# Optimization experiments

Hardware: AMD Instinct MI355X
Metric: run time of the kernel (lower is better)

## Reference

```python
import jax, jax.numpy as jnp
import numpy as np

K, N, NE, NI, MA, IN, B = 8, 512, 256, 256, 3, 128, 1024
H, UNFOLDS = 0.04, 6
DT = H / UNFOLDS
STATE = NE * MA + NI * MA + NE + NI + N  # 2560


def inv_softplus(x):
    return float(np.log(np.expm1(x)))


def piecewise_sigmoid(x, S_a=0.9, S_c=0.0):
    a = S_a / 2.0
    c = S_c
    k = 0.5 / (1.0 - 2.0 * a)  # = 5.0 for S_a=0.9
    x1, x2, x3, x4 = c + a - 1.0, c - a, c + a, c + 1.0 - a
    quad_rise = k * (x - x1) * (x - x1)
    linear = x - c + 0.5
    quad_cap = 1.0 - k * (x - x4) * (x - x4)
    out = jnp.where(x < x1, 0.0, quad_rise)
    out = jnp.where(x >= x2, linear, out)
    out = jnp.where(x > x3, quad_cap, out)
    out = jnp.where(x > x4, 1.0, out)
    return out


def setup_inputs():
    key = jax.random.key(0)
    ks = jax.random.split(key, 6)
    m = (jax.random.uniform(ks[0], (K, N, N)) > 0.5).astype(jnp.float32)  # sparsity masks
    W_raw = jax.random.normal(ks[1], (K, N, N)) * np.float32(np.sqrt(2.0 / N)) * m
    W_in = jax.random.normal(ks[2], (K, N, IN)) * 0.1
    lo, hi = inv_softplus(0.25), inv_softplus(10.0)
    taus = jnp.asarray([lo + (hi - lo) * ai / (MA - 1) for ai in range(MA)], dtype=jnp.float32)
    log_tau_a = jnp.tile(taus[None, None, :], (K, NE, 1))
    return {
        "inputs": jax.random.normal(ks[3], (B, IN), dtype=jnp.float32),
        "state": jax.random.uniform(ks[4], (K, B, STATE), dtype=jnp.float32),
        "W_raw": W_raw,
        "sparsity_masks": m,
        "W_in": W_in,
        "a_0": jnp.full((K, N), 0.35, jnp.float32),
        "log_tau_d": jnp.full((K, N), inv_softplus(0.1), jnp.float32),
        "log_tau_a_E": log_tau_a,
        "log_c_E": jnp.full((K, NE, MA), -3.0, jnp.float32),
        "c_0_E": jnp.zeros((K, NE, MA), jnp.float32),
        "log_tau_a_I": log_tau_a,
        "log_c_I": jnp.full((K, NI, MA), -3.0, jnp.float32),
        "c_0_I": jnp.zeros((K, NI, MA), jnp.float32),
        "log_tau_b_rec_E": jnp.full((K, NE), inv_softplus(1.0), jnp.float32),
        "log_tau_b_rel_E": jnp.full((K, NE), inv_softplus(0.25), jnp.float32),
        "log_tau_b_rec_I": jnp.full((K, NI), inv_softplus(1.0), jnp.float32),
        "log_tau_b_rel_I": jnp.full((K, NI), inv_softplus(0.25), jnp.float32),
        "readout_ids": jnp.zeros((K,), dtype=jnp.int32),  # 0=synaptic,1=rate,2=dendritic
    }


def _forward(inputs, state, W_raw, sparsity_masks, W_in, a_0, log_tau_d,
             log_tau_a_E, log_c_E, c_0_E, log_tau_a_I, log_c_I, c_0_I,
             log_tau_b_rec_E, log_tau_b_rel_E, log_tau_b_rec_I, log_tau_b_rel_I,
             readout_ids):
    sp = jax.nn.softplus
    # unpack flat state (K,B,STATE)
    i0 = NE * MA; i1 = i0 + NI * MA; i2 = i1 + NE; i3 = i2 + NI
    aE = state[:, :, :i0].reshape(K, B, NE, MA)
    aI = state[:, :, i0:i1].reshape(K, B, NI, MA)
    bE = state[:, :, i1:i2]          # (K,B,NE)
    bI = state[:, :, i2:i3]          # (K,B,NI)
    x = state[:, :, i3:]             # (K,B,N)
    # Dale-constrained effective recurrent weights
    W_pos = sp(W_raw)
    W_eff = jnp.concatenate([W_pos[:, :, :NE], -W_pos[:, :, NE:]], axis=2) * sparsity_masks
    # time-constant gains
    gx = DT / sp(log_tau_d)[:, None]                    # (K,1,N)
    gaE = DT / sp(log_tau_a_E)[:, None]                 # (K,1,NE,MA)
    gaI = DT / sp(log_tau_a_I)[:, None]
    cE = sp(log_c_E)[:, None]                           # (K,1,NE,MA)
    cI = sp(log_c_I)[:, None]
    grecE = (DT / sp(log_tau_b_rec_E))[:, None]         # (K,1,NE)
    grelE = (DT / sp(log_tau_b_rel_E))[:, None]
    grecI = (DT / sp(log_tau_b_rec_I))[:, None]
    grelI = (DT / sp(log_tau_b_rel_I))[:, None]
    in_cur = jnp.einsum('kni,bi->kbn', W_in, inputs)    # constant across unfolds

    def rate_syn(aE, aI, bE, bI, x):
        thr = a_0[:, None] + jnp.concatenate(
            [jnp.sum(aE + c_0_E[:, None], axis=-1),
             jnp.sum(aI + c_0_I[:, None], axis=-1)], axis=-1)
        r = piecewise_sigmoid(x - thr)                  # (K,B,N)
        s = r * jnp.concatenate([bE, bI], axis=-1)      # depression-scaled output
        return r, s

    def step(carry, _):
        aE, aI, bE, bI, x = carry
        r, s = rate_syn(aE, aI, bE, bI, x)
        rE, rI = r[..., :NE], r[..., NE:]
        syn = jnp.einsum('knm,kbm->kbn', W_eff, s) + in_cur
        x = (x + gx * syn) / (1.0 + gx)                 # semi-implicit Euler
        aE = (aE + gaE * cE * rE[..., None]) / (1.0 + gaE)
        aI = (aI + gaI * cI * rI[..., None]) / (1.0 + gaI)
        bE = (bE + grecE) / (1.0 + grecE + grelE * rE)
        bI = (bI + grecI) / (1.0 + grecI + grelI * rI)
        return (aE, aI, bE, bI, x), None

    (aE, aI, bE, bI, x), _ = jax.lax.scan(step, (aE, aI, bE, bI, x), None, length=UNFOLDS)
    r, s = rate_syn(aE, aI, bE, bI, x)
    rid = readout_ids[:, None, None]
    out = jnp.where(rid == 0, s, jnp.where(rid == 1, r, x))
    new_state = jnp.concatenate(
        [aE.reshape(K, B, -1), aI.reshape(K, B, -1), bE, bI, x], axis=-1)
    return out, new_state


def reference(inputs, state, W_raw, sparsity_masks, W_in, a_0, log_tau_d,
              log_tau_a_E, log_c_E, c_0_E, log_tau_a_I, log_c_I, c_0_I,
              log_tau_b_rec_E, log_tau_b_rel_E, log_tau_b_rec_I, log_tau_b_rel_I,
              readout_ids):
    return _forward(inputs, state, W_raw, sparsity_masks, W_in, a_0, log_tau_d,
                    log_tau_a_E, log_c_E, c_0_E, log_tau_a_I, log_c_I, c_0_I,
                    log_tau_b_rec_E, log_tau_b_rel_E, log_tau_b_rec_I, log_tau_b_rel_I,
                    readout_ids)
```

## Files before the change

### kernel.cpp

```cpp
#include <hip/hip_runtime.h>
#include <stdint.h>

#define K_ 8
#define N_ 512
#define NE_ 256
#define MA_ 3
#define IN_ 128
#define B_ 1024
#define STATE_ 2560
#define UNFOLDS_ 6
#define DT_ (0.04f / 6.0f)

typedef __attribute__((ext_vector_type(8))) short short8;
typedef __attribute__((ext_vector_type(4))) float floatx4;

__device__ __forceinline__ float b2f(uint16_t u) {
    union { uint32_t i; float f; } v; v.i = ((uint32_t)u) << 16; return v.f;
}
__device__ __forceinline__ uint16_t f2b(float f) {
    union { float f; uint32_t i; } v; v.f = f;
    uint32_t i = v.i;
    uint32_t r = i + 0x7FFFu + ((i >> 16) & 1u);
    return (uint16_t)(r >> 16);
}
__device__ __forceinline__ uint32_t pack2(uint16_t lo, uint16_t hi) {
    return (uint32_t)lo | ((uint32_t)hi << 16);
}
__device__ __forceinline__ float loadf(const void* p, size_t i, int f32) {
    return f32 ? ((const float*)p)[i] : b2f(((const uint16_t*)p)[i]);
}
__device__ __forceinline__ float spf(float x) {
    return (x > 20.f) ? x : log1pf(expf(x));
}
__device__ __forceinline__ float psig(float x) {
    float t1 = x + 0.55f;
    float q1 = 5.f * t1 * t1;
    float t2 = x - 0.55f;
    float q2 = 1.f - 5.f * t2 * t2;
    float out = (x < -0.55f) ? 0.f : q1;
    out = (x >= -0.45f) ? (x + 0.5f) : out;
    out = (x > 0.45f) ? q2 : out;
    out = (x > 0.55f) ? 1.f : out;
    return out;
}

__global__ void srnn_detect_kernel(const uint16_t* canary, int* flag) {
    __shared__ int cnt;
    if (threadIdx.x == 0) cnt = 0;
    __syncthreads();
    int bad = 0;
    for (int i = threadIdx.x; i < 4096; i += 256) {
        uint16_t u = canary[i];
        int e = (u >> 7) & 0xFF;
        if (e >= 0xC0) bad++;
    }
    atomicAdd(&cnt, bad);
    __syncthreads();
    if (threadIdx.x == 0) flag[0] = (cnt >= 16) ? 1 : 0;
}

__global__ void srnn_params_kernel(
    const void* a0, const void* ltd,
    const void* ltaE, const void* lcE, const void* c0E,
    const void* ltaI, const void* lcI, const void* c0I,
    const void* lbrecE, const void* lbrelE,
    const void* lbrecI, const void* lbrelI,
    const int* flag, float* P)
{
    const int f = flag[0];
    int idx = blockIdx.x * 256 + threadIdx.x;
    if (idx >= K_ * N_) return;
    int n = idx & (N_ - 1);
    int k = idx >> 9;
    float gx = DT_ / spf(loadf(ltd, idx, f));
    float thr0 = loadf(a0, idx, f);

    const void *lta, *lc, *c0, *lbrec, *lbrel;
    int nn;
    if (n < NE_) { nn = n;        lta = ltaE; lc = lcE; c0 = c0E; lbrec = lbrecE; lbrel = lbrelE; }
    else         { nn = n - NE_;  lta = ltaI; lc = lcI; c0 = c0I; lbrec = lbrecI; lbrel = lbrelI; }
    int base3 = (k * NE_ + nn) * MA_;
    int base1 = k * NE_ + nn;

    float amul[3], ainv[3];
    #pragma unroll
    for (int j = 0; j < 3; ++j) {
        float ga = DT_ / spf(loadf(lta, base3 + j, f));
        float c  = spf(loadf(lc, base3 + j, f));
        amul[j] = ga * c;
        ainv[j] = 1.f / (1.f + ga);
        thr0 += loadf(c0, base3 + j, f);
    }
    float grec = DT_ / spf(loadf(lbrec, base1, f));
    float grel = DT_ / spf(loadf(lbrel, base1, f));

    const int KN = K_ * N_;
    P[0*KN + idx] = gx;
    P[1*KN + idx] = 1.f / (1.f + gx);
    P[2*KN + idx] = thr0;
    P[3*KN + idx] = grec;
    P[4*KN + idx] = grel;
    P[5*KN + idx] = amul[0]; P[6*KN + idx] = amul[1]; P[7*KN + idx] = amul[2];
    P[8*KN + idx] = ainv[0]; P[9*KN + idx] = ainv[1]; P[10*KN + idx] = ainv[2];
}

__global__ __launch_bounds__(256) void srnn_wsw_kernel(
    const void* __restrict__ Wraw, const void* __restrict__ mask,
    const int* __restrict__ flag, uint16_t* __restrict__ Wsw)
{
    __shared__ float tile[16 * 516];
    const int f = flag[0];
    const int nt = blockIdx.x, k = blockIdx.y, t = threadIdx.x;
    const size_t base = (size_t)k * N_ * N_ + (size_t)nt * 16 * N_;
    #pragma unroll
    for (int i = 0; i < 32; ++i) {
        int idx = i * 256 + t;
        int row = idx >> 9, m = idx & 511;
        size_t gi = base + (size_t)row * N_ + m;
        float w = spf(loadf(Wraw, gi, f)) * loadf(mask, gi, f);
        if (m >= NE_) w = -w;
        tile[row * 516 + m] = w;
    }
    __syncthreads();
    uint16_t* outb = Wsw + ((size_t)k * 32 + nt) * (16 * 64 * 8);
    #pragma unroll
    for (int i = 0; i < 4; ++i) {
        int id = i * 256 + t;
        int ks = id >> 6, L = id & 63;
        int row = L & 15, quad = L >> 4;
        const float* src = &tile[row * 516 + ks * 32 + quad * 8];
        uint4 v;
        v.x = pack2(f2b(src[0]), f2b(src[1]));
        v.y = pack2(f2b(src[2]), f2b(src[3]));
        v.z = pack2(f2b(src[4]), f2b(src[5]));
        v.w = pack2(f2b(src[6]), f2b(src[7]));
        *(uint4*)(outb + (size_t)id * 8) = v;
    }
}

__global__ void srnn_wint_kernel(const void* Win, const int* flag, uint16_t* WinT)
{
    __shared__ float tile[32][33];
    const int f = flag[0];
    int k = blockIdx.z, nt = blockIdx.y, it = blockIdx.x;
    int tx = threadIdx.x & 31, ty = threadIdx.x >> 5;
    #pragma unroll
    for (int r = 0; r < 32; r += 8) {
        int n = nt * 32 + ty + r, i = it * 32 + tx;
        tile[ty + r][tx] = loadf(Win, ((size_t)k * N_ + n) * IN_ + i, f);
    }
    __syncthreads();
    #pragma unroll
    for (int r = 0; r < 32; r += 8) {
        int i = it * 32 + ty + r, n = nt * 32 + tx;
        WinT[((size_t)k * IN_ + i) * N_ + n] = f2b(tile[tx][ty + r]);
    }
}

__global__ __launch_bounds__(256) void srnn_ic_kernel(
    const void* __restrict__ inputs, const uint16_t* __restrict__ WinT,
    const int* __restrict__ flag, float* __restrict__ icg)
{
    __shared__ float in_lds[IN_ * 12];
    const int f = flag[0];
    const int t = threadIdx.x;
    const int k = blockIdx.y;
    const int b0 = blockIdx.x * 8;
    const int n0 = 2 * t;
    #pragma unroll
    for (int q = 0; q < 4; ++q) {
        int idx = t + q * 256;
        int bb = idx >> 7, i = idx & 127;
        in_lds[i * 12 + bb] = loadf(inputs, (size_t)(b0 + bb) * IN_ + i, f);
    }
    __syncthreads();
    float ic0[8], ic1[8];
    #pragma unroll
    for (int bb = 0; bb < 8; ++bb) { ic0[bb] = 0.f; ic1[bb] = 0.f; }
    const uint32_t* wp = (const uint32_t*)(WinT + (size_t)k * IN_ * N_);
    #pragma unroll 2
    for (int i = 0; i < IN_; ++i) {
        uint32_t w2 = wp[i * 256 + t];
        float w0 = b2f((uint16_t)w2), w1 = b2f((uint16_t)(w2 >> 16));
        const float* srow = &in_lds[i * 12];
        float s8[8];
        *(float4*)&s8[0] = *(const float4*)srow;
        *(float4*)&s8[4] = *(const float4*)(srow + 4);
        #pragma unroll
        for (int bb = 0; bb < 8; ++bb) {
            ic0[bb] = fmaf(w0, s8[bb], ic0[bb]);
            ic1[bb] = fmaf(w1, s8[bb], ic1[bb]);
        }
    }
    #pragma unroll
    for (int bb = 0; bb < 8; ++bb) {
        float2 v; v.x = ic0[bb]; v.y = ic1[bb];
        *(float2*)(icg + ((size_t)k * B_ + b0 + bb) * N_ + n0) = v;
    }
}

__global__ __launch_bounds__(512, 1)
void srnn_main_kernel(const void* __restrict__ state,
                      const uint16_t* __restrict__ Wsw,
                      const float* __restrict__ icg,
                      const float* __restrict__ P,
                      const int* __restrict__ readout,
                      const int* __restrict__ flag,
                      void* __restrict__ out)
{
    __shared__ __align__(16) uint16_t sT[16 * 520];
    __shared__ __align__(16) float synT[16 * 516];

    const int f = flag[0];
    const int t = threadIdx.x;
    const int k = blockIdx.x & 7;
    const int b0 = (blockIdx.x >> 3) * 16;
    const int n = t;
    const int lane = t & 63, w = t >> 6;
    const int bq = lane & 15, quad = lane >> 4;

    const int KN = K_ * N_;
    const int pi = k * N_ + n;
    const float gx = P[0*KN+pi], ivgx = P[1*KN+pi], thr0 = P[2*KN+pi];
    const float grec = P[3*KN+pi], grel = P[4*KN+pi];
    const float amul0 = P[5*KN+pi], amul1 = P[6*KN+pi], amul2 = P[7*KN+pi];
    const float ainv0 = P[8*KN+pi], ainv1 = P[9*KN+pi], ainv2 = P[10*KN+pi];

    float a0v[16], a1v[16], a2v[16], bv[16], xv[16], ic[16];
    #pragma unroll
    for (int bb = 0; bb < 16; ++bb) {
        size_t sb = ((size_t)k * B_ + b0 + bb) * STATE_;
        a0v[bb] = loadf(state, sb + 3 * n + 0, f);
        a1v[bb] = loadf(state, sb + 3 * n + 1, f);
        a2v[bb] = loadf(state, sb + 3 * n + 2, f);
        bv[bb]  = loadf(state, sb + 1536 + n, f);
        xv[bb]  = loadf(state, sb + 2048 + n, f);
        ic[bb]  = icg[((size_t)k * B_ + b0 + bb) * N_ + n];
    }

    const uint16_t* wbase = Wsw + (size_t)k * 32 * 16 * 64 * 8;
    const uint16_t* ape = wbase + ((size_t)(4 * w) * 16 * 64 + lane) * 8;
    const uint16_t* bpe = sT + bq * 520 + quad * 8;

    for (int step = 0; step < UNFOLDS_; ++step) {
        #pragma unroll
        for (int bb = 0; bb < 16; ++bb) {
            float thr = thr0 + a0v[bb] + a1v[bb] + a2v[bb];
            float r = psig(xv[bb] - thr);
            float s = r * bv[bb];
            a0v[bb] = fmaf(amul0, r, a0v[bb]) * ainv0;
            a1v[bb] = fmaf(amul1, r, a1v[bb]) * ainv1;
            a2v[bb] = fmaf(amul2, r, a2v[bb]) * ainv2;
            bv[bb] = (bv[bb] + grec) / (1.f + grec + grel * r);
            sT[bb * 520 + n] = f2b(s);
        }
        __syncthreads();

        floatx4 c0 = {0.f, 0.f, 0.f, 0.f}, c1 = c0, c2 = c0, c3 = c0;
        #pragma unroll 2
        for (int ks = 0; ks < 16; ++ks) {
            short8 bf = *(const short8*)(bpe + ks * 32);
            short8 af0 = *(const short8*)(ape + ks * 512);
            short8 af1 = *(const short8*)(ape + 8192 + ks * 512);
            short8 af2 = *(const short8*)(ape + 16384 + ks * 512);
            short8 af3 = *(const short8*)(ape + 24576 + ks * 512);
            c0 = __builtin_amdgcn_mfma_f32_16x16x32_bf16(af0, bf, c0, 0, 0, 0);
            c1 = __builtin_amdgcn_mfma_f32_16x16x32_bf16(af1, bf, c1, 0, 0, 0);
            c2 = __builtin_amdgcn_mfma_f32_16x16x32_bf16(af2, bf, c2, 0, 0, 0);
            c3 = __builtin_amdgcn_mfma_f32_16x16x32_bf16(af3, bf, c3, 0, 0, 0);
        }
        {
            const int nb = w * 64 + quad * 4;
            *(floatx4*)(&synT[bq * 516 + nb +  0]) = c0;
            *(floatx4*)(&synT[bq * 516 + nb + 16]) = c1;
            *(floatx4*)(&synT[bq * 516 + nb + 32]) = c2;
            *(floatx4*)(&synT[bq * 516 + nb + 48]) = c3;
        }
        __syncthreads();

        #pragma unroll
        for (int bb = 0; bb < 16; ++bb) {
            float syn = synT[bb * 516 + n] + ic[bb];
            xv[bb] = fmaf(gx, syn, xv[bb]) * ivgx;
        }
    }

    const int rid = readout[k];
    if (f) {
        float* outp = (float*)out;
        float* nst = outp + (size_t)K_ * B_ * N_;
        #pragma unroll
        for (int bb = 0; bb < 16; ++bb) {
            float thr = thr0 + a0v[bb] + a1v[bb] + a2v[bb];
            float r = psig(xv[bb] - thr);
            float s = r * bv[bb];
            float o = (rid == 0) ? s : ((rid == 1) ? r : xv[bb]);
            size_t ob = (size_t)k * B_ + b0 + bb;
            outp[ob * N_ + n] = o;
            float* st = nst + ob * STATE_;
            st[3 * n + 0] = a0v[bb];
            st[3 * n + 1] = a1v[bb];
            st[3 * n + 2] = a2v[bb];
            st[1536 + n] = bv[bb];
            st[2048 + n] = xv[bb];
        }
    } else {
        uint16_t* outp = (uint16_t*)out;
        uint16_t* nst = outp + (size_t)K_ * B_ * N_;
        #pragma unroll
        for (int bb = 0; bb < 16; ++bb) {
            float thr = thr0 + a0v[bb] + a1v[bb] + a2v[bb];
            float r = psig(xv[bb] - thr);
            float s = r * bv[bb];
            float o = (rid == 0) ? s : ((rid == 1) ? r : xv[bb]);
            size_t ob = (size_t)k * B_ + b0 + bb;
            outp[ob * N_ + n] = f2b(o);
            uint16_t* st = nst + ob * STATE_;
            st[3 * n + 0] = f2b(a0v[bb]);
            st[3 * n + 1] = f2b(a1v[bb]);
            st[3 * n + 2] = f2b(a2v[bb]);
            st[1536 + n] = f2b(bv[bb]);
            st[2048 + n] = f2b(xv[bb]);
        }
    }
}

extern "C" void kernel_launch(void* const* d_in, const int* in_sizes, int n_in,
                              void* d_out, int out_size, void* d_ws, size_t ws_size,
                              hipStream_t stream) {
    const void* inputs = d_in[0];
    const void* state  = d_in[1];
    const void* Wraw   = d_in[2];
    const void* mask   = d_in[3];
    const void* Win    = d_in[4];
    const void* a0     = d_in[5];
    const void* ltd    = d_in[6];
    const void* ltaE   = d_in[7];
    const void* lcE    = d_in[8];
    const void* c0E    = d_in[9];
    const void* ltaI   = d_in[10];
    const void* lcI    = d_in[11];
    const void* c0I    = d_in[12];
    const void* lbrecE = d_in[13];
    const void* lbrelE = d_in[14];
    const void* lbrecI = d_in[15];
    const void* lbrelI = d_in[16];
    const int* readout = (const int*)d_in[17];

    char* ws = (char*)d_ws;
    int* flag      = (int*)ws;
    float* P       = (float*)(ws + 256);
    uint16_t* Wsw  = (uint16_t*)(ws + 256 + 180224);
    uint16_t* WinT = (uint16_t*)(ws + 256 + 180224 + 4194304);
    float* icg     = (float*)(ws + 256 + 180224 + 4194304 + 1048576);

    srnn_detect_kernel<<<dim3(1), dim3(256), 0, stream>>>((const uint16_t*)Wraw, flag);
    srnn_params_kernel<<<dim3(16), dim3(256), 0, stream>>>(
        a0, ltd, ltaE, lcE, c0E, ltaI, lcI, c0I, lbrecE, lbrelE, lbrecI, lbrelI, flag, P);
    srnn_wsw_kernel<<<dim3(32, 8), dim3(256), 0, stream>>>(Wraw, mask, flag, Wsw);
    srnn_wint_kernel<<<dim3(IN_ / 32, N_ / 32, K_), dim3(256), 0, stream>>>(Win, flag, WinT);
    srnn_ic_kernel<<<dim3(B_ / 8, K_), dim3(256), 0, stream>>>(inputs, WinT, flag, icg);
    srnn_main_kernel<<<dim3(512), dim3(512), 0, stream>>>(
        state, Wsw, icg, P, readout, flag, d_out);
}
```

Before: 371.2 us.

## Fuse input projection into main kernel via MFMA and use nontemporal memory ops

Drops the separate Win transpose and scalar input-current kernels. The main kernel now computes the input current with bf16 MFMA from a swizzled Win layout and an LDS-staged input tile. This removes one launch and the icg round trip through global memory. It also adds nontemporal loads and stores for streamed data and raises the recurrent MFMA loop unroll from 2 to 4. The input current is now computed from bf16-rounded inputs and weights, which may change precision slightly, and the main kernel gains an extra prologue phase.

```diff
diff --git a/kernel.cpp b/kernel.cpp
--- a/kernel.cpp
+++ b/kernel.cpp
@@ -28,6 +28,10 @@
 }
 __device__ __forceinline__ float loadf(const void* p, size_t i, int f32) {
     return f32 ? ((const float*)p)[i] : b2f(((const uint16_t*)p)[i]);
+}
+__device__ __forceinline__ float ntloadf(const void* p, size_t i, int f32) {
+    return f32 ? __builtin_nontemporal_load((const float*)p + i)
+               : b2f(__builtin_nontemporal_load((const uint16_t*)p + i));
 }
 __device__ __forceinline__ float spf(float x) {
     return (x > 20.f) ? x : log1pf(expf(x));
@@ -117,7 +121,7 @@
         int idx = i * 256 + t;
         int row = idx >> 9, m = idx & 511;
         size_t gi = base + (size_t)row * N_ + m;
-        float w = spf(loadf(Wraw, gi, f)) * loadf(mask, gi, f);
+        float w = spf(ntloadf(Wraw, gi, f)) * ntloadf(mask, gi, f);
         if (m >= NE_) w = -w;
         tile[row * 516 + m] = w;
     }
@@ -138,71 +142,41 @@
     }
 }
 
-__global__ void srnn_wint_kernel(const void* Win, const int* flag, uint16_t* WinT)
+__global__ __launch_bounds__(256) void srnn_winsw_kernel(
+    const void* __restrict__ Win, const int* __restrict__ flag,
+    uint16_t* __restrict__ Winsw)
 {
-    __shared__ float tile[32][33];
+    __shared__ float tile[16 * 132];
     const int f = flag[0];
-    int k = blockIdx.z, nt = blockIdx.y, it = blockIdx.x;
-    int tx = threadIdx.x & 31, ty = threadIdx.x >> 5;
-    #pragma unroll
-    for (int r = 0; r < 32; r += 8) {
-        int n = nt * 32 + ty + r, i = it * 32 + tx;
-        tile[ty + r][tx] = loadf(Win, ((size_t)k * N_ + n) * IN_ + i, f);
-    }
-    __syncthreads();
-    #pragma unroll
-    for (int r = 0; r < 32; r += 8) {
-        int i = it * 32 + ty + r, n = nt * 32 + tx;
-        WinT[((size_t)k * IN_ + i) * N_ + n] = f2b(tile[tx][ty + r]);
-    }
-}
-
-__global__ __launch_bounds__(256) void srnn_ic_kernel(
-    const void* __restrict__ inputs, const uint16_t* __restrict__ WinT,
-    const int* __restrict__ flag, float* __restrict__ icg)
-{
-    __shared__ float in_lds[IN_ * 12];
-    const int f = flag[0];
-    const int t = threadIdx.x;
-    const int k = blockIdx.y;
-    const int b0 = blockIdx.x * 8;
-    const int n0 = 2 * t;
-    #pragma unroll
-    for (int q = 0; q < 4; ++q) {
-        int idx = t + q * 256;
-        int bb = idx >> 7, i = idx & 127;
-        in_lds[i * 12 + bb] = loadf(inputs, (size_t)(b0 + bb) * IN_ + i, f);
-    }
-    __syncthreads();
-    float ic0[8], ic1[8];
-    #pragma unroll
-    for (int bb = 0; bb < 8; ++bb) { ic0[bb] = 0.f; ic1[bb] = 0.f; }
-    const uint32_t* wp = (const uint32_t*)(WinT + (size_t)k * IN_ * N_);
-    #pragma unroll 2
-    for (int i = 0; i < IN_; ++i) {
-        uint32_t w2 = wp[i * 256 + t];
-        float w0 = b2f((uint16_t)w2), w1 = b2f((uint16_t)(w2 >> 16));
-        const float* srow = &in_lds[i * 12];
-        float s8[8];
-        *(float4*)&s8[0] = *(const float4*)srow;
-        *(float4*)&s8[4] = *(const float4*)(srow + 4);
-        #pragma unroll
-        for (int bb = 0; bb < 8; ++bb) {
-            ic0[bb] = fmaf(w0, s8[bb], ic0[bb]);
-            ic1[bb] = fmaf(w1, s8[bb], ic1[bb]);
-        }
-    }
-    #pragma unroll
-    for (int bb = 0; bb < 8; ++bb) {
-        float2 v; v.x = ic0[bb]; v.y = ic1[bb];
-        *(float2*)(icg + ((size_t)k * B_ + b0 + bb) * N_ + n0) = v;
+    const int nt = blockIdx.x, k = blockIdx.y, t = threadIdx.x;
+    const size_t base = (size_t)k * N_ * IN_ + (size_t)nt * 16 * IN_;
+    #pragma unroll
+    for (int i = 0; i < 8; ++i) {
+        int idx = i * 256 + t;
+        int row = idx >> 7, c = idx & 127;
+        tile[row * 132 + c] = ntloadf(Win, base + (size_t)row * IN_ + c, f);
+    }
+    __syncthreads();
+    uint16_t* outb = Winsw + ((size_t)k * 32 + nt) * (4 * 64 * 8);
+    {
+        int id = t;
+        int ks = id >> 6, L = id & 63;
+        int row = L & 15, quad = L >> 4;
+        const float* src = &tile[row * 132 + ks * 32 + quad * 8];
+        uint4 v;
+        v.x = pack2(f2b(src[0]), f2b(src[1]));
+        v.y = pack2(f2b(src[2]), f2b(src[3]));
+        v.z = pack2(f2b(src[4]), f2b(src[5]));
+        v.w = pack2(f2b(src[6]), f2b(src[7]));
+        *(uint4*)(outb + (size_t)id * 8) = v;
     }
 }
 
 __global__ __launch_bounds__(512, 1)
 void srnn_main_kernel(const void* __restrict__ state,
+                      const void* __restrict__ inputs,
                       const uint16_t* __restrict__ Wsw,
-                      const float* __restrict__ icg,
+                      const uint16_t* __restrict__ Winsw,
                       const float* __restrict__ P,
                       const int* __restrict__ readout,
                       const int* __restrict__ flag,
@@ -226,21 +200,54 @@
     const float amul0 = P[5*KN+pi], amul1 = P[6*KN+pi], amul2 = P[7*KN+pi];
     const float ainv0 = P[8*KN+pi], ainv1 = P[9*KN+pi], ainv2 = P[10*KN+pi];
 
+    #pragma unroll
+    for (int q = 0; q < 4; ++q) {
+        int idx = q * 512 + t;
+        int bb = idx >> 7, i = idx & 127;
+        sT[bb * 520 + i] = f2b(ntloadf(inputs, (size_t)(b0 + bb) * IN_ + i, f));
+    }
+
     float a0v[16], a1v[16], a2v[16], bv[16], xv[16], ic[16];
     #pragma unroll
     for (int bb = 0; bb < 16; ++bb) {
         size_t sb = ((size_t)k * B_ + b0 + bb) * STATE_;
-        a0v[bb] = loadf(state, sb + 3 * n + 0, f);
-        a1v[bb] = loadf(state, sb + 3 * n + 1, f);
-        a2v[bb] = loadf(state, sb + 3 * n + 2, f);
-        bv[bb]  = loadf(state, sb + 1536 + n, f);
-        xv[bb]  = loadf(state, sb + 2048 + n, f);
-        ic[bb]  = icg[((size_t)k * B_ + b0 + bb) * N_ + n];
-    }
-
-    const uint16_t* wbase = Wsw + (size_t)k * 32 * 16 * 64 * 8;
-    const uint16_t* ape = wbase + ((size_t)(4 * w) * 16 * 64 + lane) * 8;
+        a0v[bb] = ntloadf(state, sb + 3 * n + 0, f);
+        a1v[bb] = ntloadf(state, sb + 3 * n + 1, f);
+        a2v[bb] = ntloadf(state, sb + 3 * n + 2, f);
+        bv[bb]  = ntloadf(state, sb + 1536 + n, f);
+        xv[bb]  = ntloadf(state, sb + 2048 + n, f);
+    }
+    __syncthreads();
+
     const uint16_t* bpe = sT + bq * 520 + quad * 8;
+
+    {
+        const uint16_t* api = Winsw + ((size_t)(k * 32 + 4 * w) * 4) * 512 + (size_t)lane * 8;
+        floatx4 d0 = {0.f,0.f,0.f,0.f}, d1 = d0, d2 = d0, d3 = d0;
+        #pragma unroll
+        for (int ks = 0; ks < 4; ++ks) {
+            short8 bf = *(const short8*)(bpe + ks * 32);
+            short8 a0f = *(const short8*)(api + (0 * 4 + ks) * 512);
+            short8 a1f = *(const short8*)(api + (1 * 4 + ks) * 512);
+            short8 a2f = *(const short8*)(api + (2 * 4 + ks) * 512);
+            short8 a3f = *(const short8*)(api + (3 * 4 + ks) * 512);
+            d0 = __builtin_amdgcn_mfma_f32_16x16x32_bf16(a0f, bf, d0, 0, 0, 0);
+            d1 = __builtin_amdgcn_mfma_f32_16x16x32_bf16(a1f, bf, d1, 0, 0, 0);
+            d2 = __builtin_amdgcn_mfma_f32_16x16x32_bf16(a2f, bf, d2, 0, 0, 0);
+            d3 = __builtin_amdgcn_mfma_f32_16x16x32_bf16(a3f, bf, d3, 0, 0, 0);
+        }
+        const int nb = w * 64 + quad * 4;
+        *(floatx4*)(&synT[bq * 516 + nb +  0]) = d0;
+        *(floatx4*)(&synT[bq * 516 + nb + 16]) = d1;
+        *(floatx4*)(&synT[bq * 516 + nb + 32]) = d2;
+        *(floatx4*)(&synT[bq * 516 + nb + 48]) = d3;
+    }
+    __syncthreads();
+    #pragma unroll
+    for (int bb = 0; bb < 16; ++bb) ic[bb] = synT[bb * 516 + n];
+    __syncthreads();
+
+    const uint16_t* ape = Wsw + (size_t)k * 32 * 8192 + (size_t)(4 * w) * 8192 + (size_t)lane * 8;
 
     for (int step = 0; step < UNFOLDS_; ++step) {
         #pragma unroll
@@ -257,7 +264,7 @@
         __syncthreads();
 
         floatx4 c0 = {0.f, 0.f, 0.f, 0.f}, c1 = c0, c2 = c0, c3 = c0;
-        #pragma unroll 2
+        #pragma unroll 4
         for (int ks = 0; ks < 16; ++ks) {
             short8 bf = *(const short8*)(bpe + ks * 32);
             short8 af0 = *(const short8*)(ape + ks * 512);
@@ -296,13 +303,13 @@
             float s = r * bv[bb];
             float o = (rid == 0) ? s : ((rid == 1) ? r : xv[bb]);
             size_t ob = (size_t)k * B_ + b0 + bb;
-            outp[ob * N_ + n] = o;
+            __builtin_nontemporal_store(o, outp + ob * N_ + n);
             float* st = nst + ob * STATE_;
-            st[3 * n + 0] = a0v[bb];
-            st[3 * n + 1] = a1v[bb];
-            st[3 * n + 2] = a2v[bb];
-            st[1536 + n] = bv[bb];
-            st[2048 + n] = xv[bb];
+            __builtin_nontemporal_store(a0v[bb], st + 3 * n + 0);
+            __builtin_nontemporal_store(a1v[bb], st + 3 * n + 1);
+            __builtin_nontemporal_store(a2v[bb], st + 3 * n + 2);
+            __builtin_nontemporal_store(bv[bb], st + 1536 + n);
+            __builtin_nontemporal_store(xv[bb], st + 2048 + n);
         }
     } else {
         uint16_t* outp = (uint16_t*)out;
@@ -314,13 +321,13 @@
             float s = r * bv[bb];
             float o = (rid == 0) ? s : ((rid == 1) ? r : xv[bb]);
             size_t ob = (size_t)k * B_ + b0 + bb;
-            outp[ob * N_ + n] = f2b(o);
+            __builtin_nontemporal_store(f2b(o), outp + ob * N_ + n);
             uint16_t* st = nst + ob * STATE_;
-            st[3 * n + 0] = f2b(a0v[bb]);
-            st[3 * n + 1] = f2b(a1v[bb]);
-            st[3 * n + 2] = f2b(a2v[bb]);
-            st[1536 + n] = f2b(bv[bb]);
-            st[2048 + n] = f2b(xv[bb]);
+            __builtin_nontemporal_store(f2b(a0v[bb]), st + 3 * n + 0);
+            __builtin_nontemporal_store(f2b(a1v[bb]), st + 3 * n + 1);
+            __builtin_nontemporal_store(f2b(a2v[bb]), st + 3 * n + 2);
+            __builtin_nontemporal_store(f2b(bv[bb]), st + 1536 + n);
+            __builtin_nontemporal_store(f2b(xv[bb]), st + 2048 + n);
         }
     }
 }
@@ -348,18 +355,16 @@
     const int* readout = (const int*)d_in[17];
 
     char* ws = (char*)d_ws;
-    int* flag      = (int*)ws;
-    float* P       = (float*)(ws + 256);
-    uint16_t* Wsw  = (uint16_t*)(ws + 256 + 180224);
-    uint16_t* WinT = (uint16_t*)(ws + 256 + 180224 + 4194304);
-    float* icg     = (float*)(ws + 256 + 180224 + 4194304 + 1048576);
+    int* flag       = (int*)ws;
+    float* P        = (float*)(ws + 256);
+    uint16_t* Wsw   = (uint16_t*)(ws + 256 + 180224);
+    uint16_t* Winsw = (uint16_t*)(ws + 256 + 180224 + 4194304);
 
     srnn_detect_kernel<<<dim3(1), dim3(256), 0, stream>>>((const uint16_t*)Wraw, flag);
     srnn_params_kernel<<<dim3(16), dim3(256), 0, stream>>>(
         a0, ltd, ltaE, lcE, c0E, ltaI, lcI, c0I, lbrecE, lbrelE, lbrecI, lbrelI, flag, P);
     srnn_wsw_kernel<<<dim3(32, 8), dim3(256), 0, stream>>>(Wraw, mask, flag, Wsw);
-    srnn_wint_kernel<<<dim3(IN_ / 32, N_ / 32, K_), dim3(256), 0, stream>>>(Win, flag, WinT);
-    srnn_ic_kernel<<<dim3(B_ / 8, K_), dim3(256), 0, stream>>>(inputs, WinT, flag, icg);
+    srnn_winsw_kernel<<<dim3(32, 8), dim3(256), 0, stream>>>(Win, flag, Winsw);
     srnn_main_kernel<<<dim3(512), dim3(512), 0, stream>>>(
-        state, Wsw, icg, P, readout, flag, d_out);
-}
+        state, inputs, Wsw, Winsw, P, readout, flag, d_out);
+}
```

Measured after the change: 343.8 us. 1.08x faster.
